# Optimization experiments

Measured on AMD Instinct MI355X. Metric: run time of the kernel, lower is better.

Reference implementation:

```python
import jax, jax.numpy as jnp
import numpy as np

B, T, IN, H, OUT = 256, 100, 128, 1024, 35
BITS = 4
SLOPE = 25.0
THR_H = 1.0
THR_O = 1.0
BETA1, BETA2, BETA3, BETA4 = 0.9, 0.85, 0.8, 0.95


def fake_quant(w, w_min, w_max, bits=BITS):
    # FakeQuantize in training mode: STE -> forward value is quantized, grad passes through clamp
    levels = 2 ** bits
    scale = (w_max - w_min) / (levels - 1)
    wc = jnp.clip(w, w_min, w_max)
    q = jnp.round((wc - w_min) / scale) * scale + w_min
    return wc + jax.lax.stop_gradient(q - wc)


@jax.custom_vjp
def spike(x):
    # Heaviside forward, fast-sigmoid surrogate backward (snn.surrogate.fast_sigmoid)
    return (x > 0).astype(x.dtype)

def _spike_fwd(x):
    return (x > 0).astype(x.dtype), x

def _spike_bwd(x, g):
    return (g / (SLOPE * jnp.abs(x) + 1.0) ** 2,)

spike.defvjp(_spike_fwd, _spike_bwd)


def lif_step(cur, mem, beta, thr, reset_mechanism):
    # snntorch Leaky (reset_delay semantics): reset computed from previous mem, detached
    reset = jax.lax.stop_gradient((mem > thr).astype(cur.dtype))
    base = beta * mem + cur
    if reset_mechanism == "subtract":
        mem_new = base - reset * thr
    else:  # "zero"
        mem_new = base - reset * base
    spk = spike(mem_new - thr)
    return spk, mem_new


def setup_inputs() -> dict:
    key = jax.random.key(0)
    ks = jax.random.split(key, 5)
    x = jax.random.normal(ks[0], (B, T, IN), dtype=jnp.float32)
    # QuantLinear init: uniform(w_min, w_max); fc1 uses (-0.5, 0.5), others (0.001, 1.0)
    w1 = jax.random.uniform(ks[1], (H, IN), minval=-0.5, maxval=0.5, dtype=jnp.float32)
    w2 = jax.random.uniform(ks[2], (H, H), minval=0.001, maxval=1.0, dtype=jnp.float32)
    w3 = jax.random.uniform(ks[3], (H, H), minval=0.001, maxval=1.0, dtype=jnp.float32)
    w4 = jax.random.uniform(ks[4], (OUT, H), minval=0.001, maxval=1.0, dtype=jnp.float32)
    return {"x": x, "w1": w1, "w2": w2, "w3": w3, "w4": w4}


def reference(x, w1, w2, w3, w4):
    # hoist weight quantization out of the time loop (identical math each step)
    q1 = fake_quant(w1, -0.5, 0.5)
    q2 = fake_quant(w2, 0.001, 1.0)
    q3 = fake_quant(w3, 0.001, 1.0)
    q4 = fake_quant(w4, 0.001, 1.0)
    xs = jnp.transpose(x, (1, 0, 2)) / 15.0  # [T, B, IN]
    Bx = x.shape[0]

    def step(carry, xt):
        m1, m2, m3, m4 = carry
        s1, m1 = lif_step(xt @ q1.T, m1, BETA1, THR_H, "subtract")
        s2, m2 = lif_step(s1 @ q2.T, m2, BETA2, THR_H, "subtract")
        s3, m3 = lif_step(s2 @ q3.T, m3, BETA3, THR_H, "subtract")
        s4, m4 = lif_step(s3 @ q4.T, m4, BETA4, THR_O, "zero")
        return (m1, m2, m3, m4), (s1, s2, s3, s4, m4)

    init = (jnp.zeros((Bx, H), x.dtype), jnp.zeros((Bx, H), x.dtype),
            jnp.zeros((Bx, H), x.dtype), jnp.zeros((Bx, OUT), x.dtype))
    _, (spk1, spk2, spk3, spk4, mem4) = jax.lax.scan(step, init, xs)
    # stacked along time dim 0, matching torch.stack(dim=0)
    return spk1, spk2, spk3, spk4, mem4
```

## Files before the change

kernel.cpp:

```cpp
#include <hip/hip_runtime.h>
#include <stdint.h>

#define NB  256
#define NT  100
#define NIN 128
#define NH  1024
#define NOUT 35
#define MT  112

#define O_SPK2 26214400ull
#define O_SPK3 52428800ull
#define O_SPK4 78643200ull
#define O_MEM4 79539200ull

#define WS_SPK0 0ull
#define WS_SPK1 29360128ull
#define WS_K2B  58720256ull
#define WS_K3B  59768832ull
#define WS_K4B  60817408ull
#define WS_Q1T  60866560ull
#define WS_N1   61390848ull
#define WS_N2   61493248ull
#define WS_N3   61595648ull

#define S2C ((float)((1.0 - 0.001) / 15.0))
#define S1C ((float)(1.0 / 15.0))

typedef int v4i __attribute__((ext_vector_type(4)));

__device__ __forceinline__ void async16(const void* g, void* l) {
  __builtin_amdgcn_global_load_lds((const __attribute__((address_space(1))) uint32_t*)g,
                                   (__attribute__((address_space(3))) uint32_t*)l, 16, 0, 0);
}

__device__ __forceinline__ uint8_t qk(float w) {
  float wc = fminf(fmaxf(w, 0.001f), 1.0f);
  return (uint8_t)(int)rintf((wc - 0.001f) / S2C);
}

__global__ void k_prep(const float* __restrict__ w1, const float* __restrict__ w2,
                       const float* __restrict__ w3, const float* __restrict__ w4,
                       uint8_t* __restrict__ ws)
{
  long long id = (long long)blockIdx.x * 256 + threadIdx.x;
  if (id < 1048576) { ws[WS_K2B + id] = qk(w2[id]); return; }
  id -= 1048576;
  if (id < 1048576) { ws[WS_K3B + id] = qk(w3[id]); return; }
  id -= 1048576;
  if (id < 49152) {
    int j = (int)(id >> 10), i = (int)(id & 1023);
    ws[WS_K4B + id] = (j < NOUT) ? qk(w4[(size_t)j * 1024 + i]) : (uint8_t)0;
    return;
  }
  id -= 49152;
  if (id < 131072) {
    int i = (int)(id >> 10), j = (int)(id & 1023);
    float wv = w1[(size_t)j * 128 + i];
    float wc = fminf(fmaxf(wv, -0.5f), 0.5f);
    float q = rintf((wc + 0.5f) / S1C) * S1C - 0.5f;
    ((float*)(ws + WS_Q1T))[id] = q;
    return;
  }
  id -= 131072;
  if (id < 76800) ((uint32_t*)(ws + WS_N1))[id] = 0;
}

__global__ __launch_bounds__(256) void k_cur1(const float* __restrict__ x,
                                              const uint8_t* __restrict__ ws,
                                              float* __restrict__ out)
{
  __shared__ float xsT[128 * 68];
  __shared__ float qch[16 * 256];
  const float* q1T = (const float*)(ws + WS_Q1T);
  const int tid = threadIdx.x;
  const int rb = blockIdx.x >> 2, cb = blockIdx.x & 3;
  const int t = rb >> 2, b0 = (rb & 3) * 64;
  const int jI = tid & 63, rI = tid >> 6;
  const int j4 = jI * 4, r16 = rI * 16;

  #pragma unroll
  for (int k = 0; k < 32; ++k) {
    int e = tid + k * 256;
    int r = e >> 7, i = e & 127;
    xsT[i * 68 + r] = x[((size_t)(b0 + r) * NT + t) * NIN + i] / 15.0f;
  }
  float acc[16][4];
  #pragma unroll
  for (int d = 0; d < 16; ++d) { acc[d][0]=0.f; acc[d][1]=0.f; acc[d][2]=0.f; acc[d][3]=0.f; }
  for (int ic = 0; ic < 8; ++ic) {
    __syncthreads();
    #pragma unroll
    for (int k = 0; k < 16; ++k) {
      int e = tid + k * 256;
      int ii = e >> 8, j = e & 255;
      qch[ii * 256 + j] = q1T[((size_t)(ic * 16 + ii) << 10) + cb * 256 + j];
    }
    __syncthreads();
    #pragma unroll
    for (int ii = 0; ii < 16; ++ii) {
      int i = ic * 16 + ii;
      const float4 q  = *(const float4*)&qch[ii * 256 + j4];
      const float4 xa = *(const float4*)&xsT[i * 68 + r16];
      const float4 xb = *(const float4*)&xsT[i * 68 + r16 + 4];
      const float4 xc = *(const float4*)&xsT[i * 68 + r16 + 8];
      const float4 xd = *(const float4*)&xsT[i * 68 + r16 + 12];
      float xr[16];
      xr[0]=xa.x; xr[1]=xa.y; xr[2]=xa.z; xr[3]=xa.w;
      xr[4]=xb.x; xr[5]=xb.y; xr[6]=xb.z; xr[7]=xb.w;
      xr[8]=xc.x; xr[9]=xc.y; xr[10]=xc.z; xr[11]=xc.w;
      xr[12]=xd.x; xr[13]=xd.y; xr[14]=xd.z; xr[15]=xd.w;
      #pragma unroll
      for (int d = 0; d < 16; ++d) {
        acc[d][0] = fmaf(xr[d], q.x, acc[d][0]);
        acc[d][1] = fmaf(xr[d], q.y, acc[d][1]);
        acc[d][2] = fmaf(xr[d], q.z, acc[d][2]);
        acc[d][3] = fmaf(xr[d], q.w, acc[d][3]);
      }
    }
  }
  #pragma unroll
  for (int d = 0; d < 16; ++d) {
    float4 v = make_float4(acc[d][0], acc[d][1], acc[d][2], acc[d][3]);
    *(float4*)&out[((size_t)rb * 64 + r16 + d) * 1024 + cb * 256 + j4] = v;
  }
}

__global__ __launch_bounds__(256) void k_scan1(uint8_t* __restrict__ ws, float* __restrict__ out)
{
  const int tid = threadIdx.x;
  const int b = blockIdx.x >> 2;
  const int j = (blockIdx.x & 3) * 256 + tid;
  uint8_t* spk0 = ws + WS_SPK0;
  uint32_t* n1 = (uint32_t*)(ws + WS_N1);
  const size_t stride = (size_t)NB * NH;
  size_t idx = (size_t)b * NH + j;
  size_t sidx = (size_t)b * MT * 1024 + j;
  float m = 0.f;
  float c = out[idx];
  for (int t = 0; t < NT; ++t) {
    float cn = (t + 1 < NT) ? out[idx + stride] : 0.f;
    float rst = m > 1.0f ? 1.0f : 0.0f;
    m = fmaf(0.9f, m, c) - rst;
    bool sp = (m - 1.0f) > 0.0f;
    out[idx] = sp ? 1.0f : 0.0f;
    spk0[sidx] = sp ? 1 : 0;
    unsigned long long bal = __ballot(sp);
    if ((tid & 63) == 0) atomicAdd((unsigned int*)&n1[t * NB + b], (unsigned)__popcll(bal));
    idx += stride; sidx += 1024; c = cn;
  }
  for (int t = NT; t < MT; ++t) { spk0[sidx] = 0; sidx += 1024; }
}

__global__ __launch_bounds__(256) void k_l23(const uint8_t* __restrict__ Aspk,
                                             const uint8_t* __restrict__ Bq,
                                             const uint32_t* __restrict__ nprev,
                                             uint32_t* __restrict__ nout,
                                             float beta,
                                             float* __restrict__ outF,
                                             uint8_t* __restrict__ spkOut)
{
  __shared__ uint8_t lds[61440];
  __shared__ uint32_t nbuf[112];
  uint8_t* sA = lds;
  uint8_t* sB = lds + 28672;
  uint16_t* cbuf = (uint16_t*)lds;

  const int b = blockIdx.x, jb = blockIdx.y;
  const int tid = threadIdx.x, lane = tid & 63, wave = tid >> 6;
  const int lm = lane & 15, lk = lane >> 4;

  if (tid < NT) nbuf[tid] = nprev[tid * NB + b];

  const uint8_t* Ab = Aspk + (size_t)b * MT * 1024;
  const uint8_t* Bb = Bq + (size_t)jb * 128 * 1024;

  v4i acc[7][2];
  #pragma unroll
  for (int m = 0; m < 7; ++m)
    #pragma unroll
    for (int n = 0; n < 2; ++n) { acc[m][n][0]=0; acc[m][n][1]=0; acc[m][n][2]=0; acc[m][n][3]=0; }

  for (int kk = 0; kk < 1024; kk += 256) {
    __syncthreads();
    #pragma unroll
    for (int q = 0; q < 15; ++q) {
      int cid = wave * 15 + q;
      if (cid < 28) {
        int mt = cid >> 2, ks = cid & 3;
        async16(Ab + (size_t)(mt * 16 + lm) * 1024 + kk + ks * 64 + lk * 16, sA + cid * 1024);
      } else if (cid < 60) {
        int c2 = cid - 28, nt = c2 >> 2, ks = c2 & 3;
        async16(Bb + (size_t)(nt * 16 + lm) * 1024 + kk + ks * 64 + lk * 16, sB + c2 * 1024);
      }
    }
    __syncthreads();
    #pragma unroll
    for (int ks = 0; ks < 4; ++ks) {
      v4i bv0 = *(const v4i*)(sB + (size_t)((2 * wave) * 4 + ks) * 1024 + lane * 16);
      v4i bv1 = *(const v4i*)(sB + (size_t)((2 * wave + 1) * 4 + ks) * 1024 + lane * 16);
      #pragma unroll
      for (int m = 0; m < 7; ++m) {
        v4i av = *(const v4i*)(sA + (size_t)(m * 4 + ks) * 1024 + lane * 16);
        acc[m][0] = __builtin_amdgcn_mfma_i32_16x16x64_i8(av, bv0, acc[m][0], 0, 0, 0);
        acc[m][1] = __builtin_amdgcn_mfma_i32_16x16x64_i8(av, bv1, acc[m][1], 0, 0, 0);
      }
    }
  }
  __syncthreads();
  #pragma unroll
  for (int m = 0; m < 7; ++m)
    #pragma unroll
    for (int n = 0; n < 2; ++n)
      #pragma unroll
      for (int r = 0; r < 4; ++r) {
        int row = m * 16 + lk * 4 + r;
        int col = (2 * wave + n) * 16 + lm;
        cbuf[row * 132 + col] = (uint16_t)acc[m][n][r];
      }
  __syncthreads();

  if (tid < 128) {
    int j = tid;
    float m = 0.f;
    for (int t = 0; t < NT; ++t) {
      int kv = cbuf[t * 132 + j];
      float cur = fmaf(S2C, (float)kv, 0.001f * (float)nbuf[t]);
      float rst = m > 1.0f ? 1.0f : 0.0f;
      m = fmaf(beta, m, cur) - rst;
      bool sp = (m - 1.0f) > 0.0f;
      outF[((size_t)t * NB + b) * NH + jb * 128 + j] = sp ? 1.0f : 0.0f;
      spkOut[((size_t)b * MT + t) * 1024 + jb * 128 + j] = sp ? 1 : 0;
      unsigned long long bal = __ballot(sp);
      if ((tid & 63) == 0) atomicAdd((unsigned int*)&nout[t * NB + b], (unsigned)__popcll(bal));
    }
    for (int t = NT; t < MT; ++t)
      spkOut[((size_t)b * MT + t) * 1024 + jb * 128 + j] = 0;
  }
}

__global__ __launch_bounds__(256) void k_l4(const uint8_t* __restrict__ Aspk,
                                            const uint8_t* __restrict__ ws,
                                            float* __restrict__ out)
{
  __shared__ uint8_t lds[40960];
  __shared__ uint32_t nbuf[112];
  uint8_t* sA = lds;
  uint8_t* sB = lds + 28672;
  uint16_t* cbuf = (uint16_t*)lds;

  const int b = blockIdx.x;
  const int tid = threadIdx.x, lane = tid & 63, wave = tid >> 6;
  const int lm = lane & 15, lk = lane >> 4;
  const uint8_t* Bq = ws + WS_K4B;
  const uint32_t* n3 = (const uint32_t*)(ws + WS_N3);

  if (tid < NT) nbuf[tid] = n3[tid * NB + b];

  const uint8_t* Ab = Aspk + (size_t)b * MT * 1024;

  v4i acc[7];
  #pragma unroll
  for (int m = 0; m < 7; ++m) { acc[m][0]=0; acc[m][1]=0; acc[m][2]=0; acc[m][3]=0; }

  for (int kk = 0; kk < 1024; kk += 256) {
    __syncthreads();
    #pragma unroll
    for (int q = 0; q < 10; ++q) {
      int cid = wave * 10 + q;
      if (cid < 28) {
        int mt = cid >> 2, ks = cid & 3;
        async16(Ab + (size_t)(mt * 16 + lm) * 1024 + kk + ks * 64 + lk * 16, sA + cid * 1024);
      } else if (cid < 40) {
        int c2 = cid - 28, nt = c2 >> 2, ks = c2 & 3;
        async16(Bq + (size_t)(nt * 16 + lm) * 1024 + kk + ks * 64 + lk * 16, sB + c2 * 1024);
      }
    }
    __syncthreads();
    if (wave < 3) {
      #pragma unroll
      for (int ks = 0; ks < 4; ++ks) {
        v4i bv = *(const v4i*)(sB + (size_t)(wave * 4 + ks) * 1024 + lane * 16);
        #pragma unroll
        for (int m = 0; m < 7; ++m) {
          v4i av = *(const v4i*)(sA + (size_t)(m * 4 + ks) * 1024 + lane * 16);
          acc[m] = __builtin_amdgcn_mfma_i32_16x16x64_i8(av, bv, acc[m], 0, 0, 0);
        }
      }
    }
  }
  __syncthreads();
  if (wave < 3) {
    #pragma unroll
    for (int m = 0; m < 7; ++m)
      #pragma unroll
      for (int r = 0; r < 4; ++r) {
        int row = m * 16 + lk * 4 + r;
        int col = wave * 16 + lm;
        cbuf[row * 52 + col] = (uint16_t)acc[m][r];
      }
  }
  __syncthreads();

  if (tid < NOUT) {
    int j = tid;
    float m = 0.f;
    for (int t = 0; t < NT; ++t) {
      int kv = cbuf[t * 52 + j];
      float cur = fmaf(S2C, (float)kv, 0.001f * (float)nbuf[t]);
      float rst = m > 1.0f ? 1.0f : 0.0f;
      float bsv = fmaf(0.95f, m, cur);
      m = (rst > 0.0f) ? 0.0f : bsv;
      size_t rowO = ((size_t)t * NB + b) * NOUT + j;
      out[O_SPK4 + rowO] = ((m - 1.0f) > 0.0f) ? 1.0f : 0.0f;
      out[O_MEM4 + rowO] = m;
    }
  }
}

extern "C" void kernel_launch(void* const* d_in, const int* in_sizes, int n_in,
                              void* d_out, int out_size, void* d_ws, size_t ws_size,
                              hipStream_t stream)
{
  const float* x  = (const float*)d_in[0];
  const float* w1 = (const float*)d_in[1];
  const float* w2 = (const float*)d_in[2];
  const float* w3 = (const float*)d_in[3];
  const float* w4 = (const float*)d_in[4];
  float* out = (float*)d_out;
  uint8_t* ws = (uint8_t*)d_ws;

  uint8_t* SPK0 = ws + WS_SPK0;
  uint8_t* SPK1 = ws + WS_SPK1;
  uint32_t* N1 = (uint32_t*)(ws + WS_N1);
  uint32_t* N2 = (uint32_t*)(ws + WS_N2);
  uint32_t* N3 = (uint32_t*)(ws + WS_N3);

  hipLaunchKernelGGL(k_prep, dim3(9196), dim3(256), 0, stream, w1, w2, w3, w4, ws);
  hipLaunchKernelGGL(k_cur1, dim3(1600), dim3(256), 0, stream, x, ws, out);
  hipLaunchKernelGGL(k_scan1, dim3(1024), dim3(256), 0, stream, ws, out);
  hipLaunchKernelGGL(k_l23, dim3(256, 8), dim3(256), 0, stream,
                     SPK0, ws + WS_K2B, N1, N2, 0.85f, out + O_SPK2, SPK1);
  hipLaunchKernelGGL(k_l23, dim3(256, 8), dim3(256), 0, stream,
                     SPK1, ws + WS_K3B, N2, N3, 0.8f, out + O_SPK3, SPK0);
  hipLaunchKernelGGL(k_l4,  dim3(256), dim3(256), 0, stream, SPK0, ws, out);
}
```

Baseline: 727.5 us.

## Fuse layers 2-4 into one per-batch kernel with double-buffered staging

Replaces the two k_l23 launches and k_l4 with a single kernel, one block per batch row, that runs layers 2, 3 and 4 in sequence. Spike counts move from global atomics into LDS counters. The K loop now uses double-buffered async LDS staging in 128-wide chunks, and the scan reads packed 16-bit currents into registers. The aim is to cut launch and inter-kernel sync overhead and global atomics. In exchange the grid shrinks from 2048 blocks to 256, one block per CU, so parallelism and latency hiding drop.

```diff
diff --git a/kernel.cpp b/kernel.cpp
--- a/kernel.cpp
+++ b/kernel.cpp
@@ -20,8 +20,6 @@
 #define WS_K4B  60817408ull
 #define WS_Q1T  60866560ull
 #define WS_N1   61390848ull
-#define WS_N2   61493248ull
-#define WS_N3   61595648ull
 
 #define S2C ((float)((1.0 - 0.001) / 15.0))
 #define S1C ((float)(1.0 / 15.0))
@@ -62,7 +60,7 @@
     return;
   }
   id -= 131072;
-  if (id < 76800) ((uint32_t*)(ws + WS_N1))[id] = 0;
+  if (id < 25600) ((uint32_t*)(ws + WS_N1))[id] = 0;
 }
 
 __global__ __launch_bounds__(256) void k_cur1(const float* __restrict__ x,
@@ -151,168 +149,180 @@
   for (int t = NT; t < MT; ++t) { spk0[sidx] = 0; sidx += 1024; }
 }
 
-__global__ __launch_bounds__(256) void k_l23(const uint8_t* __restrict__ Aspk,
-                                             const uint8_t* __restrict__ Bq,
-                                             const uint32_t* __restrict__ nprev,
-                                             uint32_t* __restrict__ nout,
-                                             float beta,
-                                             float* __restrict__ outF,
-                                             uint8_t* __restrict__ spkOut)
-{
-  __shared__ uint8_t lds[61440];
-  __shared__ uint32_t nbuf[112];
-  uint8_t* sA = lds;
-  uint8_t* sB = lds + 28672;
-  uint16_t* cbuf = (uint16_t*)lds;
-
-  const int b = blockIdx.x, jb = blockIdx.y;
-  const int tid = threadIdx.x, lane = tid & 63, wave = tid >> 6;
-  const int lm = lane & 15, lk = lane >> 4;
-
-  if (tid < NT) nbuf[tid] = nprev[tid * NB + b];
-
-  const uint8_t* Ab = Aspk + (size_t)b * MT * 1024;
-  const uint8_t* Bb = Bq + (size_t)jb * 128 * 1024;
-
-  v4i acc[7][2];
-  #pragma unroll
-  for (int m = 0; m < 7; ++m)
-    #pragma unroll
-    for (int n = 0; n < 2; ++n) { acc[m][n][0]=0; acc[m][n][1]=0; acc[m][n][2]=0; acc[m][n][3]=0; }
-
-  for (int kk = 0; kk < 1024; kk += 256) {
-    __syncthreads();
-    #pragma unroll
-    for (int q = 0; q < 15; ++q) {
-      int cid = wave * 15 + q;
-      if (cid < 28) {
-        int mt = cid >> 2, ks = cid & 3;
-        async16(Ab + (size_t)(mt * 16 + lm) * 1024 + kk + ks * 64 + lk * 16, sA + cid * 1024);
-      } else if (cid < 60) {
-        int c2 = cid - 28, nt = c2 >> 2, ks = c2 & 3;
-        async16(Bb + (size_t)(nt * 16 + lm) * 1024 + kk + ks * 64 + lk * 16, sB + c2 * 1024);
-      }
-    }
-    __syncthreads();
-    #pragma unroll
-    for (int ks = 0; ks < 4; ++ks) {
-      v4i bv0 = *(const v4i*)(sB + (size_t)((2 * wave) * 4 + ks) * 1024 + lane * 16);
-      v4i bv1 = *(const v4i*)(sB + (size_t)((2 * wave + 1) * 4 + ks) * 1024 + lane * 16);
-      #pragma unroll
-      for (int m = 0; m < 7; ++m) {
-        v4i av = *(const v4i*)(sA + (size_t)(m * 4 + ks) * 1024 + lane * 16);
-        acc[m][0] = __builtin_amdgcn_mfma_i32_16x16x64_i8(av, bv0, acc[m][0], 0, 0, 0);
-        acc[m][1] = __builtin_amdgcn_mfma_i32_16x16x64_i8(av, bv1, acc[m][1], 0, 0, 0);
-      }
-    }
-  }
-  __syncthreads();
-  #pragma unroll
-  for (int m = 0; m < 7; ++m)
-    #pragma unroll
-    for (int n = 0; n < 2; ++n)
-      #pragma unroll
-      for (int r = 0; r < 4; ++r) {
-        int row = m * 16 + lk * 4 + r;
-        int col = (2 * wave + n) * 16 + lm;
-        cbuf[row * 132 + col] = (uint16_t)acc[m][n][r];
-      }
-  __syncthreads();
-
-  if (tid < 128) {
-    int j = tid;
-    float m = 0.f;
-    for (int t = 0; t < NT; ++t) {
-      int kv = cbuf[t * 132 + j];
-      float cur = fmaf(S2C, (float)kv, 0.001f * (float)nbuf[t]);
-      float rst = m > 1.0f ? 1.0f : 0.0f;
-      m = fmaf(beta, m, cur) - rst;
-      bool sp = (m - 1.0f) > 0.0f;
-      outF[((size_t)t * NB + b) * NH + jb * 128 + j] = sp ? 1.0f : 0.0f;
-      spkOut[((size_t)b * MT + t) * 1024 + jb * 128 + j] = sp ? 1 : 0;
-      unsigned long long bal = __ballot(sp);
-      if ((tid & 63) == 0) atomicAdd((unsigned int*)&nout[t * NB + b], (unsigned)__popcll(bal));
-    }
-    for (int t = NT; t < MT; ++t)
-      spkOut[((size_t)b * MT + t) * 1024 + jb * 128 + j] = 0;
-  }
-}
-
-__global__ __launch_bounds__(256) void k_l4(const uint8_t* __restrict__ Aspk,
-                                            const uint8_t* __restrict__ ws,
-                                            float* __restrict__ out)
-{
-  __shared__ uint8_t lds[40960];
-  __shared__ uint32_t nbuf[112];
-  uint8_t* sA = lds;
-  uint8_t* sB = lds + 28672;
-  uint16_t* cbuf = (uint16_t*)lds;
+__global__ __launch_bounds__(256, 1) void k_l234(uint8_t* __restrict__ ws, float* __restrict__ out)
+{
+  __shared__ __align__(16) uint8_t lds[91328];
+  uint8_t*  sAB     = lds;
+  uint16_t* cbuf16  = (uint16_t*)(lds + 61440);
+  uint16_t* nprev16 = (uint16_t*)(lds + 90624);
+  uint32_t* nnextL  = (uint32_t*)(lds + 90880);
 
   const int b = blockIdx.x;
   const int tid = threadIdx.x, lane = tid & 63, wave = tid >> 6;
   const int lm = lane & 15, lk = lane >> 4;
-  const uint8_t* Bq = ws + WS_K4B;
-  const uint32_t* n3 = (const uint32_t*)(ws + WS_N3);
-
-  if (tid < NT) nbuf[tid] = n3[tid * NB + b];
-
-  const uint8_t* Ab = Aspk + (size_t)b * MT * 1024;
-
-  v4i acc[7];
-  #pragma unroll
-  for (int m = 0; m < 7; ++m) { acc[m][0]=0; acc[m][1]=0; acc[m][2]=0; acc[m][3]=0; }
-
-  for (int kk = 0; kk < 1024; kk += 256) {
-    __syncthreads();
+
+  uint8_t* SPK0b = ws + WS_SPK0 + (size_t)b * MT * 1024;
+  uint8_t* SPK1b = ws + WS_SPK1 + (size_t)b * MT * 1024;
+  const uint32_t* n1g = (const uint32_t*)(ws + WS_N1);
+
+  if (tid < NT) nprev16[tid] = (uint16_t)n1g[tid * NB + b];
+  if (tid >= NT && tid < MT) nprev16[tid] = 0;
+  if (tid < MT) nnextL[tid] = 0;
+
+  auto stage = [&](int p, const uint8_t* Ab, const uint8_t* Bb, int ng, int kc, int nB) {
+    uint8_t* base = sAB + p * 30720;
     #pragma unroll
-    for (int q = 0; q < 10; ++q) {
-      int cid = wave * 10 + q;
-      if (cid < 28) {
-        int mt = cid >> 2, ks = cid & 3;
-        async16(Ab + (size_t)(mt * 16 + lm) * 1024 + kk + ks * 64 + lk * 16, sA + cid * 1024);
-      } else if (cid < 40) {
-        int c2 = cid - 28, nt = c2 >> 2, ks = c2 & 3;
-        async16(Bq + (size_t)(nt * 16 + lm) * 1024 + kk + ks * 64 + lk * 16, sB + c2 * 1024);
-      }
+    for (int q = 0; q < 8; ++q) {
+      int cid = wave * 8 + q;
+      if (cid < 14) {
+        int mt = cid >> 1, kh = cid & 1;
+        async16(Ab + (size_t)(mt * 16 + lm) * 1024 + kc * 128 + kh * 64 + lk * 16,
+                base + cid * 1024);
+      } else if (cid < 14 + nB) {
+        int c2 = cid - 14, nt = c2 >> 1, kh = c2 & 1;
+        async16(Bb + (size_t)(ng * 128 + nt * 16 + lm) * 1024 + kc * 128 + kh * 64 + lk * 16,
+                base + cid * 1024);
+      }
+    }
+  };
+
+  auto hidden = [&](const uint8_t* Ab, const uint8_t* Bb, float* outF,
+                    uint8_t* spkN, float beta) {
+    stage(0, Ab, Bb, 0, 0, 16);
+    int p = 0;
+    for (int ng = 0; ng < 8; ++ng) {
+      v4i acc[7][2];
+      #pragma unroll
+      for (int m = 0; m < 7; ++m)
+        #pragma unroll
+        for (int n = 0; n < 2; ++n) { acc[m][n][0]=0; acc[m][n][1]=0; acc[m][n][2]=0; acc[m][n][3]=0; }
+      for (int kc = 0; kc < 8; ++kc) {
+        __syncthreads();
+        if (kc < 7)      stage(p ^ 1, Ab, Bb, ng, kc + 1, 16);
+        else if (ng < 7) stage(p ^ 1, Ab, Bb, ng + 1, 0, 16);
+        const uint8_t* base = sAB + p * 30720;
+        #pragma unroll
+        for (int ks = 0; ks < 2; ++ks) {
+          v4i bv0 = *(const v4i*)(base + (size_t)(14 + (2 * wave) * 2 + ks) * 1024 + lane * 16);
+          v4i bv1 = *(const v4i*)(base + (size_t)(14 + (2 * wave + 1) * 2 + ks) * 1024 + lane * 16);
+          #pragma unroll
+          for (int m = 0; m < 7; ++m) {
+            v4i av = *(const v4i*)(base + (size_t)(m * 2 + ks) * 1024 + lane * 16);
+            acc[m][0] = __builtin_amdgcn_mfma_i32_16x16x64_i8(av, bv0, acc[m][0], 0, 0, 0);
+            acc[m][1] = __builtin_amdgcn_mfma_i32_16x16x64_i8(av, bv1, acc[m][1], 0, 0, 0);
+          }
+        }
+        p ^= 1;
+      }
+      __syncthreads();
+      #pragma unroll
+      for (int m = 0; m < 7; ++m)
+        #pragma unroll
+        for (int n = 0; n < 2; ++n) {
+          int col = (2 * wave + n) * 16 + lm;
+          int row = m * 16 + lk * 4;
+          uint32_t v01 = (uint32_t)(acc[m][n][0] & 0xffff) | ((uint32_t)acc[m][n][1] << 16);
+          uint32_t v23 = (uint32_t)(acc[m][n][2] & 0xffff) | ((uint32_t)acc[m][n][3] << 16);
+          *(uint32_t*)&cbuf16[col * 114 + row]     = v01;
+          *(uint32_t*)&cbuf16[col * 114 + row + 2] = v23;
+        }
+      __syncthreads();
+      if (tid < 128) {
+        int j = tid;
+        uint32_t cr[50], nr[50];
+        #pragma unroll
+        for (int q = 0; q < 50; ++q) cr[q] = *(const uint32_t*)&cbuf16[j * 114 + 2 * q];
+        #pragma unroll
+        for (int q = 0; q < 50; ++q) nr[q] = *(const uint32_t*)&nprev16[2 * q];
+        float m = 0.f;
+        #pragma unroll
+        for (int t = 0; t < NT; ++t) {
+          uint32_t kv = (t & 1) ? (cr[t >> 1] >> 16) : (cr[t >> 1] & 0xffffu);
+          uint32_t nv = (t & 1) ? (nr[t >> 1] >> 16) : (nr[t >> 1] & 0xffffu);
+          float cur = fmaf(S2C, (float)kv, 0.001f * (float)nv);
+          float rst = m > 1.0f ? 1.0f : 0.0f;
+          m = fmaf(beta, m, cur) - rst;
+          bool sp = (m - 1.0f) > 0.0f;
+          __builtin_nontemporal_store(sp ? 1.0f : 0.0f,
+              &outF[((size_t)t * NB + b) * NH + ng * 128 + j]);
+          spkN[(size_t)t * 1024 + ng * 128 + j] = sp ? 1 : 0;
+          unsigned long long bal = __ballot(sp);
+          if (lane == 0) atomicAdd((unsigned int*)&nnextL[t], (unsigned)__popcll(bal));
+        }
+        #pragma unroll
+        for (int t = NT; t < MT; ++t)
+          spkN[(size_t)t * 1024 + ng * 128 + j] = 0;
+      }
+    }
+  };
+
+  hidden(SPK0b, ws + WS_K2B, out + O_SPK2, SPK1b, 0.85f);
+  __syncthreads();
+  if (tid < MT) { nprev16[tid] = (uint16_t)nnextL[tid]; nnextL[tid] = 0; }
+  __syncthreads();
+  hidden(SPK1b, ws + WS_K3B, out + O_SPK3, SPK0b, 0.8f);
+  __syncthreads();
+  if (tid < MT) { nprev16[tid] = (uint16_t)nnextL[tid]; }
+  __syncthreads();
+
+  {
+    const uint8_t* Ab = SPK0b;
+    const uint8_t* Bb = ws + WS_K4B;
+    v4i acc[7];
+    #pragma unroll
+    for (int m = 0; m < 7; ++m) { acc[m][0]=0; acc[m][1]=0; acc[m][2]=0; acc[m][3]=0; }
+    stage(0, Ab, Bb, 0, 0, 6);
+    int p = 0;
+    for (int kc = 0; kc < 8; ++kc) {
+      __syncthreads();
+      if (kc < 7) stage(p ^ 1, Ab, Bb, 0, kc + 1, 6);
+      const uint8_t* base = sAB + p * 30720;
+      if (wave < 3) {
+        #pragma unroll
+        for (int ks = 0; ks < 2; ++ks) {
+          v4i bv = *(const v4i*)(base + (size_t)(14 + wave * 2 + ks) * 1024 + lane * 16);
+          #pragma unroll
+          for (int m = 0; m < 7; ++m) {
+            v4i av = *(const v4i*)(base + (size_t)(m * 2 + ks) * 1024 + lane * 16);
+            acc[m] = __builtin_amdgcn_mfma_i32_16x16x64_i8(av, bv, acc[m], 0, 0, 0);
+          }
+        }
+      }
+      p ^= 1;
     }
     __syncthreads();
     if (wave < 3) {
       #pragma unroll
-      for (int ks = 0; ks < 4; ++ks) {
-        v4i bv = *(const v4i*)(sB + (size_t)(wave * 4 + ks) * 1024 + lane * 16);
-        #pragma unroll
-        for (int m = 0; m < 7; ++m) {
-          v4i av = *(const v4i*)(sA + (size_t)(m * 4 + ks) * 1024 + lane * 16);
-          acc[m] = __builtin_amdgcn_mfma_i32_16x16x64_i8(av, bv, acc[m], 0, 0, 0);
-        }
-      }
-    }
-  }
-  __syncthreads();
-  if (wave < 3) {
-    #pragma unroll
-    for (int m = 0; m < 7; ++m)
-      #pragma unroll
-      for (int r = 0; r < 4; ++r) {
-        int row = m * 16 + lk * 4 + r;
+      for (int m = 0; m < 7; ++m) {
         int col = wave * 16 + lm;
-        cbuf[row * 52 + col] = (uint16_t)acc[m][r];
-      }
-  }
-  __syncthreads();
-
-  if (tid < NOUT) {
-    int j = tid;
-    float m = 0.f;
-    for (int t = 0; t < NT; ++t) {
-      int kv = cbuf[t * 52 + j];
-      float cur = fmaf(S2C, (float)kv, 0.001f * (float)nbuf[t]);
-      float rst = m > 1.0f ? 1.0f : 0.0f;
-      float bsv = fmaf(0.95f, m, cur);
-      m = (rst > 0.0f) ? 0.0f : bsv;
-      size_t rowO = ((size_t)t * NB + b) * NOUT + j;
-      out[O_SPK4 + rowO] = ((m - 1.0f) > 0.0f) ? 1.0f : 0.0f;
-      out[O_MEM4 + rowO] = m;
+        int row = m * 16 + lk * 4;
+        uint32_t v01 = (uint32_t)(acc[m][0] & 0xffff) | ((uint32_t)acc[m][1] << 16);
+        uint32_t v23 = (uint32_t)(acc[m][2] & 0xffff) | ((uint32_t)acc[m][3] << 16);
+        *(uint32_t*)&cbuf16[col * 114 + row]     = v01;
+        *(uint32_t*)&cbuf16[col * 114 + row + 2] = v23;
+      }
+    }
+    __syncthreads();
+    if (tid < NOUT) {
+      int j = tid;
+      uint32_t cr[50], nr[50];
+      #pragma unroll
+      for (int q = 0; q < 50; ++q) cr[q] = *(const uint32_t*)&cbuf16[j * 114 + 2 * q];
+      #pragma unroll
+      for (int q = 0; q < 50; ++q) nr[q] = *(const uint32_t*)&nprev16[2 * q];
+      float m = 0.f;
+      #pragma unroll
+      for (int t = 0; t < NT; ++t) {
+        uint32_t kv = (t & 1) ? (cr[t >> 1] >> 16) : (cr[t >> 1] & 0xffffu);
+        uint32_t nv = (t & 1) ? (nr[t >> 1] >> 16) : (nr[t >> 1] & 0xffffu);
+        float cur = fmaf(S2C, (float)kv, 0.001f * (float)nv);
+        float rst = m > 1.0f ? 1.0f : 0.0f;
+        float bsv = fmaf(0.95f, m, cur);
+        m = (rst > 0.0f) ? 0.0f : bsv;
+        size_t rowO = ((size_t)t * NB + b) * NOUT + j;
+        __builtin_nontemporal_store(((m - 1.0f) > 0.0f) ? 1.0f : 0.0f, &out[O_SPK4 + rowO]);
+        __builtin_nontemporal_store(m, &out[O_MEM4 + rowO]);
+      }
     }
   }
 }
@@ -329,18 +339,8 @@
   float* out = (float*)d_out;
   uint8_t* ws = (uint8_t*)d_ws;
 
-  uint8_t* SPK0 = ws + WS_SPK0;
-  uint8_t* SPK1 = ws + WS_SPK1;
-  uint32_t* N1 = (uint32_t*)(ws + WS_N1);
-  uint32_t* N2 = (uint32_t*)(ws + WS_N2);
-  uint32_t* N3 = (uint32_t*)(ws + WS_N3);
-
-  hipLaunchKernelGGL(k_prep, dim3(9196), dim3(256), 0, stream, w1, w2, w3, w4, ws);
+  hipLaunchKernelGGL(k_prep, dim3(9096), dim3(256), 0, stream, w1, w2, w3, w4, ws);
   hipLaunchKernelGGL(k_cur1, dim3(1600), dim3(256), 0, stream, x, ws, out);
   hipLaunchKernelGGL(k_scan1, dim3(1024), dim3(256), 0, stream, ws, out);
-  hipLaunchKernelGGL(k_l23, dim3(256, 8), dim3(256), 0, stream,
-                     SPK0, ws + WS_K2B, N1, N2, 0.85f, out + O_SPK2, SPK1);
-  hipLaunchKernelGGL(k_l23, dim3(256, 8), dim3(256), 0, stream,
-                     SPK1, ws + WS_K3B, N2, N3, 0.8f, out + O_SPK3, SPK0);
-  hipLaunchKernelGGL(k_l4,  dim3(256), dim3(256), 0, stream, SPK0, ws, out);
-}
+  hipLaunchKernelGGL(k_l234, dim3(256), dim3(256), 0, stream, ws, out);
+}
```

Result: slower. 859.9 us (+18.2%).
